# Optimization experiments

Hardware: AMD Instinct MI355X
Metric: run time of the kernel (lower is better)

## Reference

```python
import jax, jax.numpy as jnp
import numpy as np


def setup_inputs() -> dict:
    key = jax.random.key(0)
    ks = jax.random.split(key, 9)
    I, J, H, B = 1024, 1024, 32, 1024
    hid = 10
    d_in = 3 + 3 * H  # 99
    return {
        "X": jax.random.normal(ks[0], (B, I), dtype=jnp.float32),
        "weight": jax.random.normal(ks[1], (I, J), dtype=jnp.float32) * 0.1,
        "hidden_state": jax.random.normal(ks[2], (I, J, H), dtype=jnp.float32) * 0.1,
        "W1": jax.random.normal(ks[3], (d_in, hid), dtype=jnp.float32) / np.sqrt(d_in),
        "b1": jax.random.normal(ks[4], (hid,), dtype=jnp.float32) * 0.01,
        "W2": jax.random.normal(ks[5], (hid, hid), dtype=jnp.float32) / np.sqrt(hid),
        "b2": jax.random.normal(ks[6], (hid,), dtype=jnp.float32) * 0.01,
        "W3": jax.random.normal(ks[7], (hid, 1 + H), dtype=jnp.float32) / np.sqrt(hid),
        "b3": jax.random.normal(ks[8], (1 + H,), dtype=jnp.float32) * 0.01,
    }


def reference(X, weight, hidden_state, W1, b1, W2, b2, W3, b3):
    I, J = weight.shape
    H = hidden_state.shape[-1]
    # Leave-one-out means, computed once via full sums (the original recomputes
    # slice+concat+mean per cell in nested Python loops: O(I*J*(I+J)) work).
    fwd_w = (jnp.sum(weight, axis=0, keepdims=True) - weight) / (I - 1)  # (I,J) col mean excl. row i
    bwd_w = (jnp.sum(weight, axis=1, keepdims=True) - weight) / (J - 1)  # (I,J) row mean excl. col j
    fwd_h = (jnp.sum(hidden_state, axis=0, keepdims=True) - hidden_state) / (I - 1)  # (I,J,H)
    bwd_h = (jnp.sum(hidden_state, axis=1, keepdims=True) - hidden_state) / (J - 1)  # (I,J,H)
    # Per-cell feature: [w_ij, mean_fwd_w, mean_bwd_w, h_ij, mean_fwd_h, mean_bwd_h] -> (I,J,3+3H)
    feat = jnp.concatenate(
        [weight[..., None], fwd_w[..., None], bwd_w[..., None], hidden_state, fwd_h, bwd_h],
        axis=-1,
    )
    # Tiny 3-layer MLP batched over all cells (local_nn).
    h = jax.nn.relu(feat @ W1 + b1)
    h = jax.nn.relu(h @ W2 + b2)
    upd = h @ W3 + b3  # (I,J,1+H)
    new_weight = weight + upd[..., 0]
    new_hidden = hidden_state + upd[..., 1:]
    probs = jax.nn.softmax(X @ new_weight, axis=-1)  # (B,J)
    return probs, new_weight, new_hidden
```

## Files before the change

kernel.cpp:

```cpp
#include <hip/hip_runtime.h>

#define INV_I1 (1.0f/1023.0f)
#define INV_J1 (1.0f/1023.0f)

#define WS_CW     0
#define WS_RW     1024
#define WS_CH     2048
#define WS_PJT    34816
#define WS_QI     45056
#define WS_CST    55296
#define WS_LOGITS 65536
#define WS_RHP    65536
#define WS_WCP    327680
#define WS_HPART  344064

typedef __attribute__((ext_vector_type(8))) short bf16x8;
typedef __attribute__((ext_vector_type(4))) float f32x4;

__device__ inline ushort bf16_rne(float x) {
  union { float f; unsigned u; } v; v.f = x;
  unsigned r = v.u + 0x7fffu + ((v.u >> 16) & 1u);
  return (ushort)(r >> 16);
}
__device__ inline float bf16_tof(ushort h) {
  union { unsigned u; float f; } c; c.u = ((unsigned)h) << 16;
  return c.f;
}

__global__ __launch_bounds__(512) void k_red1(const float* __restrict__ Hd,
                                              float* __restrict__ hpart,
                                              float* __restrict__ rhpart,
                                              int npart) {
  __shared__ float4 s4[512];
  int t = threadIdx.x;
  int wv = t >> 6, lane = t & 63;
  int p = blockIdx.x >> 3, c = blockIdx.x & 7;
  int R = 1024 / npart;
  int i0 = p * R;
  float4 ca0 = make_float4(0.f,0.f,0.f,0.f);
  float4 ca1 = make_float4(0.f,0.f,0.f,0.f);
  for (int g = 0; g < R; g += 8) {
    #pragma unroll
    for (int r = 0; r < 8; r++) {
      int i = i0 + g + r;
      const float4* rowc = (const float4*)(Hd + (size_t)i * 32768 + c * 4096);
      float4 v0 = rowc[t];
      float4 v1 = rowc[t + 512];
      ca0.x += v0.x; ca0.y += v0.y; ca0.z += v0.z; ca0.w += v0.w;
      ca1.x += v1.x; ca1.y += v1.y; ca1.z += v1.z; ca1.w += v1.w;
      float4 rs;
      rs.x = v0.x + v1.x; rs.y = v0.y + v1.y;
      rs.z = v0.z + v1.z; rs.w = v0.w + v1.w;
      #pragma unroll
      for (int off = 8; off <= 32; off <<= 1) {
        rs.x += __shfl_xor(rs.x, off, 64);
        rs.y += __shfl_xor(rs.y, off, 64);
        rs.z += __shfl_xor(rs.z, off, 64);
        rs.w += __shfl_xor(rs.w, off, 64);
      }
      if (lane < 8) s4[(r * 8 + wv) * 8 + lane] = rs;
    }
    __syncthreads();
    if (t < 64) {
      int r = t >> 3, ln = t & 7;
      float4 a = s4[(r * 8 + 0) * 8 + ln];
      #pragma unroll
      for (int w2 = 1; w2 < 8; w2++) {
        float4 b = s4[(r * 8 + w2) * 8 + ln];
        a.x += b.x; a.y += b.y; a.z += b.z; a.w += b.w;
      }
      int i = i0 + g + r;
      ((float4*)rhpart)[i * 64 + c * 8 + ln] = a;
    }
    __syncthreads();
  }
  float4* hp = (float4*)(hpart + (size_t)p * 32768 + c * 4096);
  hp[t] = ca0;
  hp[t + 512] = ca1;
}

__global__ __launch_bounds__(256) void k_wred(const float* __restrict__ W,
                                              const float* __restrict__ X,
                                              float* __restrict__ ws,
                                              float* __restrict__ wcp,
                                              ushort* __restrict__ Xb) {
  int b = blockIdx.x, t = threadIdx.x;
  if (b < 128) {
    int wv = t >> 6, lane = t & 63;
    #pragma unroll
    for (int rr = 0; rr < 2; rr++) {
      int row = b * 8 + wv * 2 + rr;
      float acc = 0.f;
      #pragma unroll
      for (int m = 0; m < 16; m++) acc += W[row * 1024 + lane + 64 * m];
      #pragma unroll
      for (int off = 32; off > 0; off >>= 1) acc += __shfl_down(acc, off, 64);
      if (lane == 0) ws[WS_RW + row] = acc;
    }
  } else if (b < 144) {
    int p = b - 128;
    float a0 = 0.f, a1 = 0.f, a2 = 0.f, a3 = 0.f;
    for (int i = p * 64; i < p * 64 + 64; i++) {
      const float* row = W + (size_t)i * 1024;
      a0 += row[t]; a1 += row[t + 256]; a2 += row[t + 512]; a3 += row[t + 768];
    }
    wcp[p * 1024 + t] = a0;       wcp[p * 1024 + t + 256] = a1;
    wcp[p * 1024 + t + 512] = a2; wcp[p * 1024 + t + 768] = a3;
  } else {
    int g = (b - 144) * 256 + t;
    float4 v0 = ((const float4*)X)[g * 2];
    float4 v1 = ((const float4*)X)[g * 2 + 1];
    float xs[8] = {v0.x, v0.y, v0.z, v0.w, v1.x, v1.y, v1.z, v1.w};
    ushort hi[8], lo[8];
    #pragma unroll
    for (int e = 0; e < 8; e++) {
      hi[e] = bf16_rne(xs[e]);
      lo[e] = bf16_rne(xs[e] - bf16_tof(hi[e]));
    }
    ((uint4*)Xb)[g] = *(uint4*)hi;
    ((uint4*)(Xb + 1048576))[g] = *(uint4*)lo;
  }
}

__global__ __launch_bounds__(256) void k_red2pq(const float* __restrict__ hpart,
                                                const float* __restrict__ wcp,
                                                const float* __restrict__ rhpart,
                                                const float* __restrict__ W1,
                                                const float* __restrict__ b1,
                                                const float* __restrict__ W2,
                                                const float* __restrict__ b2,
                                                const float* __restrict__ W3,
                                                const float* __restrict__ b3,
                                                float* __restrict__ ws, int npart) {
  int b = blockIdx.x, t = threadIdx.x;
  if (b < 128) {
    __shared__ float chl[256];
    __shared__ float cwl[8];
    int col = b * 256 + t;
    float acc = 0.f;
    for (int p = 0; p < npart; p++) acc += hpart[(size_t)p * 32768 + col];
    ws[WS_CH + col] = acc;
    chl[t] = acc;
    if (t < 8) {
      int j = b * 8 + t;
      float a = 0.f;
      #pragma unroll
      for (int p = 0; p < 16; p++) a += wcp[p * 1024 + j];
      ws[WS_CW + j] = a;
      cwl[t] = a;
    }
    __syncthreads();
    if (t < 80) {
      int jj = t / 10, q = t - jj * 10;
      int j = b * 8 + jj;
      float o = cwl[jj] * INV_I1 * W1[10 + q];
      for (int k = 0; k < 32; k++)
        o += chl[jj * 32 + k] * INV_I1 * W1[(35 + k) * 10 + q];
      ws[WS_PJT + q * 1024 + j] = o;
    }
  } else if (b < 132) {
    int i = (b - 128) * 256 + t;
    float rh[32];
    #pragma unroll
    for (int k = 0; k < 32; k++) rh[k] = 0.f;
    for (int c = 0; c < 8; c++) {
      #pragma unroll
      for (int k = 0; k < 32; k++) rh[k] += rhpart[i * 256 + c * 32 + k];
    }
    float sr = ws[WS_RW + i] * INV_J1;
    float out[10];
    #pragma unroll
    for (int q = 0; q < 10; q++) out[q] = b1[q] + sr * W1[20 + q];
    for (int k = 0; k < 32; k++) {
      float cc = rh[k] * INV_J1;
      #pragma unroll
      for (int q = 0; q < 10; q++) out[q] += cc * W1[(67 + k) * 10 + q];
    }
    #pragma unroll
    for (int q = 0; q < 10; q++) ws[WS_QI + i * 10 + q] = out[q];
  } else {
    for (int idx = t; idx < 330; idx += 256) {
      int r = idx / 10, q = idx - r * 10;
      float v;
      if (r == 0)
        v = W1[q] - W1[10 + q] * INV_I1 - W1[20 + q] * INV_J1;
      else
        v = W1[(2 + r) * 10 + q] - W1[(34 + r) * 10 + q] * INV_I1 - W1[(66 + r) * 10 + q] * INV_J1;
      ws[WS_CST + idx] = v;
    }
    for (int idx = t; idx < 100; idx += 256) ws[WS_CST + 330 + idx] = W2[idx];
    for (int idx = t; idx < 330; idx += 256) {
      int o = idx / 10, q2 = idx - o * 10;
      ws[WS_CST + 430 + idx] = W3[q2 * 33 + o];
    }
    if (t < 10) ws[WS_CST + 760 + t] = b2[t];
    if (t < 33) ws[WS_CST + 770 + t] = b3[t];
  }
}

__global__ __launch_bounds__(256) void k_mlp(
    const float* __restrict__ W, const float* __restrict__ Hd,
    const float* __restrict__ ws,
    float* __restrict__ newW, float* __restrict__ newH) {
  __shared__ __align__(16) float hbuf[8192];
  int t = threadIdx.x;
  int cell0 = blockIdx.x * 256;
  int i = blockIdx.x >> 2;
  int j0 = (blockIdx.x & 3) * 256;
  const float* cst = ws + WS_CST;

  const float4* src = (const float4*)(Hd + (size_t)cell0 * 32);
  #pragma unroll
  for (int m = 0; m < 8; m++) {
    int s = t + 256 * m;
    float4 v = src[s];
    int cs = s >> 3, ms = s & 7;
    int slot = cs * 8 + ((ms + cs) & 7);
    *(float4*)&hbuf[slot * 4] = v;
  }
  float w0 = W[cell0 + t];
  float pj[10];
  #pragma unroll
  for (int q = 0; q < 10; q++) pj[q] = ws[WS_PJT + q * 1024 + j0 + t];
  float qv[10];
  #pragma unroll
  for (int q = 0; q < 10; q++) qv[q] = ws[WS_QI + i * 10 + q];
  __syncthreads();

  float h[32];
  #pragma unroll
  for (int m = 0; m < 8; m++) {
    int slot = t * 8 + ((m + t) & 7);
    float4 v = *(const float4*)&hbuf[slot * 4];
    h[m * 4 + 0] = v.x; h[m * 4 + 1] = v.y; h[m * 4 + 2] = v.z; h[m * 4 + 3] = v.w;
  }

  float z[10];
  #pragma unroll
  for (int q = 0; q < 10; q++) z[q] = pj[q] + qv[q] + w0 * cst[q];
  #pragma unroll
  for (int k = 0; k < 32; k++) {
    #pragma unroll
    for (int q = 0; q < 10; q++) z[q] += h[k] * cst[(k + 1) * 10 + q];
  }
  #pragma unroll
  for (int q = 0; q < 10; q++) z[q] = fmaxf(z[q], 0.f);

  float y[10];
  #pragma unroll
  for (int q2 = 0; q2 < 10; q2++) y[q2] = cst[760 + q2];
  #pragma unroll
  for (int q = 0; q < 10; q++) {
    #pragma unroll
    for (int q2 = 0; q2 < 10; q2++) y[q2] += z[q] * cst[330 + q * 10 + q2];
  }
  #pragma unroll
  for (int q2 = 0; q2 < 10; q2++) y[q2] = fmaxf(y[q2], 0.f);

  float u = cst[770];
  #pragma unroll
  for (int q2 = 0; q2 < 10; q2++) u += y[q2] * cst[430 + q2];
  newW[cell0 + t] = w0 + u;

  #pragma unroll
  for (int o = 1; o < 33; o++) {
    float a = cst[770 + o];
    #pragma unroll
    for (int q2 = 0; q2 < 10; q2++) a += y[q2] * cst[430 + o * 10 + q2];
    h[o - 1] += a;
  }

  #pragma unroll
  for (int m = 0; m < 8; m++) {
    int slot = t * 8 + ((m + t) & 7);
    *(float4*)&hbuf[slot * 4] = make_float4(h[m * 4], h[m * 4 + 1], h[m * 4 + 2], h[m * 4 + 3]);
  }
  __syncthreads();
  float4* dst = (float4*)(newH + (size_t)cell0 * 32);
  #pragma unroll
  for (int m = 0; m < 8; m++) {
    int s = t + 256 * m;
    int cs = s >> 3, ms = s & 7;
    int slot = cs * 8 + ((ms + cs) & 7);
    dst[s] = *(const float4*)&hbuf[slot * 4];
  }
}

__global__ __launch_bounds__(256) void k_wt(const float* __restrict__ nW,
                                            ushort* __restrict__ Wt) {
  __shared__ float buf[64][65];
  int t = threadIdx.x;
  int i0 = blockIdx.y * 64, j0 = blockIdx.x * 64;
  int jl = t & 63, rr = t >> 6;
  #pragma unroll
  for (int r2 = 0; r2 < 16; r2++) {
    int il = r2 * 4 + rr;
    buf[jl][il] = nW[(size_t)(i0 + il) * 1024 + j0 + jl];
  }
  __syncthreads();
  int jw = t >> 2, iq = (t & 3) * 16;
  ushort hi[16], lo[16];
  #pragma unroll
  for (int e = 0; e < 16; e++) {
    float x = buf[jw][iq + e];
    ushort h = bf16_rne(x);
    hi[e] = h;
    lo[e] = bf16_rne(x - bf16_tof(h));
  }
  size_t base = (size_t)(j0 + jw) * 1024 + i0 + iq;
  *(uint4*)(Wt + base)     = *(uint4*)hi;
  *(uint4*)(Wt + base + 8) = *(uint4*)(hi + 8);
  *(uint4*)(Wt + 1048576 + base)     = *(uint4*)lo;
  *(uint4*)(Wt + 1048576 + base + 8) = *(uint4*)(lo + 8);
}

__global__ __launch_bounds__(256) void k_gemm(const ushort* __restrict__ Xb,
                                              const ushort* __restrict__ Wt,
                                              float* __restrict__ C) {
  int t = threadIdx.x;
  int w = t >> 6, l = t & 63;
  int m0 = blockIdx.y * 64 + (w >> 1) * 32;
  int n0 = blockIdx.x * 64 + (w & 1) * 32;
  int lr = l & 15;
  int kg = (l >> 4) * 8;
  const ushort* Xhi = Xb;
  const ushort* Xlo = Xb + 1048576;
  const ushort* Whi = Wt;
  const ushort* Wlo = Wt + 1048576;
  const size_t ra0 = (size_t)(m0 + lr) * 1024;
  const size_t ra1 = (size_t)(m0 + 16 + lr) * 1024;
  const size_t cb0 = (size_t)(n0 + lr) * 1024;
  const size_t cb1 = (size_t)(n0 + 16 + lr) * 1024;
  f32x4 acc00 = {0.f, 0.f, 0.f, 0.f};
  f32x4 acc01 = {0.f, 0.f, 0.f, 0.f};
  f32x4 acc10 = {0.f, 0.f, 0.f, 0.f};
  f32x4 acc11 = {0.f, 0.f, 0.f, 0.f};
  #pragma unroll 2
  for (int k0 = 0; k0 < 1024; k0 += 32) {
    int o = k0 + kg;
    bf16x8 ah0 = *(const bf16x8*)(Xhi + ra0 + o);
    bf16x8 ah1 = *(const bf16x8*)(Xhi + ra1 + o);
    bf16x8 al0 = *(const bf16x8*)(Xlo + ra0 + o);
    bf16x8 al1 = *(const bf16x8*)(Xlo + ra1 + o);
    bf16x8 bh0 = *(const bf16x8*)(Whi + cb0 + o);
    bf16x8 bh1 = *(const bf16x8*)(Whi + cb1 + o);
    bf16x8 bl0 = *(const bf16x8*)(Wlo + cb0 + o);
    bf16x8 bl1 = *(const bf16x8*)(Wlo + cb1 + o);
    acc00 = __builtin_amdgcn_mfma_f32_16x16x32_bf16(ah0, bh0, acc00, 0, 0, 0);
    acc01 = __builtin_amdgcn_mfma_f32_16x16x32_bf16(ah0, bh1, acc01, 0, 0, 0);
    acc10 = __builtin_amdgcn_mfma_f32_16x16x32_bf16(ah1, bh0, acc10, 0, 0, 0);
    acc11 = __builtin_amdgcn_mfma_f32_16x16x32_bf16(ah1, bh1, acc11, 0, 0, 0);
    acc00 = __builtin_amdgcn_mfma_f32_16x16x32_bf16(ah0, bl0, acc00, 0, 0, 0);
    acc01 = __builtin_amdgcn_mfma_f32_16x16x32_bf16(ah0, bl1, acc01, 0, 0, 0);
    acc10 = __builtin_amdgcn_mfma_f32_16x16x32_bf16(ah1, bl0, acc10, 0, 0, 0);
    acc11 = __builtin_amdgcn_mfma_f32_16x16x32_bf16(ah1, bl1, acc11, 0, 0, 0);
    acc00 = __builtin_amdgcn_mfma_f32_16x16x32_bf16(al0, bh0, acc00, 0, 0, 0);
    acc01 = __builtin_amdgcn_mfma_f32_16x16x32_bf16(al0, bh1, acc01, 0, 0, 0);
    acc10 = __builtin_amdgcn_mfma_f32_16x16x32_bf16(al1, bh0, acc10, 0, 0, 0);
    acc11 = __builtin_amdgcn_mfma_f32_16x16x32_bf16(al1, bh1, acc11, 0, 0, 0);
  }
  int rbase = m0 + (l >> 4) * 4;
  #pragma unroll
  for (int r = 0; r < 4; r++) {
    C[(size_t)(rbase + r) * 1024 + n0 + lr]           = acc00[r];
    C[(size_t)(rbase + r) * 1024 + n0 + 16 + lr]      = acc01[r];
    C[(size_t)(rbase + 16 + r) * 1024 + n0 + lr]      = acc10[r];
    C[(size_t)(rbase + 16 + r) * 1024 + n0 + 16 + lr] = acc11[r];
  }
}

__global__ __launch_bounds__(256) void k_softmax(const float* __restrict__ L,
                                                 float* __restrict__ P) {
  __shared__ float sm[4], ss[4];
  int r = blockIdx.x, t = threadIdx.x;
  const float* row = L + r * 1024;
  float v0 = row[t], v1 = row[t + 256], v2 = row[t + 512], v3 = row[t + 768];
  float m = fmaxf(fmaxf(v0, v1), fmaxf(v2, v3));
  #pragma unroll
  for (int off = 32; off > 0; off >>= 1) m = fmaxf(m, __shfl_xor(m, off, 64));
  int wv = t >> 6, lane = t & 63;
  if (lane == 0) sm[wv] = m;
  __syncthreads();
  m = fmaxf(fmaxf(sm[0], sm[1]), fmaxf(sm[2], sm[3]));
  float e0 = expf(v0 - m), e1 = expf(v1 - m), e2 = expf(v2 - m), e3 = expf(v3 - m);
  float s = e0 + e1 + e2 + e3;
  #pragma unroll
  for (int off = 32; off > 0; off >>= 1) s += __shfl_xor(s, off, 64);
  if (lane == 0) ss[wv] = s;
  __syncthreads();
  s = ss[0] + ss[1] + ss[2] + ss[3];
  float inv = 1.0f / s;
  float* prow = P + r * 1024;
  prow[t] = e0 * inv; prow[t + 256] = e1 * inv;
  prow[t + 512] = e2 * inv; prow[t + 768] = e3 * inv;
}

extern "C" void kernel_launch(void* const* d_in, const int* in_sizes, int n_in,
                              void* d_out, int out_size, void* d_ws, size_t ws_size,
                              hipStream_t stream) {
  const float* X  = (const float*)d_in[0];
  const float* W  = (const float*)d_in[1];
  const float* Hd = (const float*)d_in[2];
  const float* W1 = (const float*)d_in[3];
  const float* b1 = (const float*)d_in[4];
  const float* W2 = (const float*)d_in[5];
  const float* b2 = (const float*)d_in[6];
  const float* W3 = (const float*)d_in[7];
  const float* b3 = (const float*)d_in[8];
  float* out   = (float*)d_out;
  float* probs = out;
  float* newW  = out + 1024 * 1024;
  float* newH  = out + 2 * 1024 * 1024;
  float* ws = (float*)d_ws;

  size_t wsf = ws_size / 4;
  int npart = 64;
  while (npart > 8 &&
         (size_t)WS_HPART + (size_t)npart * 32768ull + 2097152ull > wsf)
    npart >>= 1;
  float*  rhpart = ws + WS_RHP;
  float*  wcp    = ws + WS_WCP;
  float*  hpart  = ws + WS_HPART;
  size_t  xb0    = (size_t)WS_HPART + (size_t)npart * 32768ull;
  ushort* Xb     = (ushort*)(ws + xb0);
  ushort* Wt     = (ushort*)(ws + xb0 + 1048576);

  k_red1<<<npart * 8, 512, 0, stream>>>(Hd, hpart, rhpart, npart);
  k_wred<<<656, 256, 0, stream>>>(W, X, ws, wcp, Xb);
  k_red2pq<<<133, 256, 0, stream>>>(hpart, wcp, rhpart, W1, b1, W2, b2, W3, b3,
                                    ws, npart);
  k_mlp<<<4096, 256, 0, stream>>>(W, Hd, ws, newW, newH);
  k_wt<<<dim3(16, 16), 256, 0, stream>>>(newW, Wt);
  k_gemm<<<dim3(16, 16), 256, 0, stream>>>(Xb, Wt, ws + WS_LOGITS);
  k_softmax<<<1024, 256, 0, stream>>>(ws + WS_LOGITS, probs);
}
```

Measured before the change: 157.1 us.

## Fuse all stages into one cooperative persistent kernel with grid syncs

Replaces the seven-kernel pipeline with a single cooperative kernel of 512 blocks that runs reductions, MLP, transpose, GEMM and softmax in phases separated by grid.sync. The aim is to remove per-kernel launch gaps and tail effects between the many small stages. In exchange the kernel is capped at 512 blocks, which changes the work split of each phase (for example, the GEMM tiles shrink to 32x64 and the MLP loops over 8 tiles per block). Grid barriers also add sync cost. The previous multi-kernel path stays as a fallback when cooperative launch is not possible.

```diff
diff --git a/kernel.cpp b/kernel.cpp
--- a/kernel.cpp
+++ b/kernel.cpp
@@ -1,4 +1,7 @@
 #include <hip/hip_runtime.h>
+#include <hip/hip_cooperative_groups.h>
+
+namespace cg = cooperative_groups;
 
 #define INV_I1 (1.0f/1023.0f)
 #define INV_J1 (1.0f/1023.0f)
@@ -9,10 +12,14 @@
 #define WS_PJT    34816
 #define WS_QI     45056
 #define WS_CST    55296
-#define WS_LOGITS 65536
-#define WS_RHP    65536
-#define WS_WCP    327680
-#define WS_HPART  344064
+#define MG_RHP    65536
+#define MG_WCP    327680
+#define MG_HPART  344064
+#define MG_LOGITS 344064
+#define MG_WT     1392640
+#define MG_XB     2441216
+#define MG_TOTAL  3489792
+#define FB_LOGITS 65536
 
 typedef __attribute__((ext_vector_type(8))) short bf16x8;
 typedef __attribute__((ext_vector_type(4))) float f32x4;
@@ -25,6 +32,369 @@
 __device__ inline float bf16_tof(ushort h) {
   union { unsigned u; float f; } c; c.u = ((unsigned)h) << 16;
   return c.f;
+}
+
+__global__ __launch_bounds__(256, 2) void mega(
+    const float* __restrict__ X, const float* __restrict__ W,
+    const float* __restrict__ Hd, const float* __restrict__ W1,
+    const float* __restrict__ b1, const float* __restrict__ W2,
+    const float* __restrict__ b2, const float* __restrict__ W3,
+    const float* __restrict__ b3, float* __restrict__ out,
+    float* __restrict__ ws) {
+  __shared__ __align__(16) float smem[8192];
+  cg::grid_group grid = cg::this_grid();
+  const int blk = blockIdx.x;
+  const int t = threadIdx.x;
+  const int wv = t >> 6, lane = t & 63;
+
+  float* probs = out;
+  float* newW  = out + 1048576;
+  float* newH  = out + 2097152;
+  float* rhpart = ws + MG_RHP;
+  float* wcp    = ws + MG_WCP;
+  float* hpart  = ws + MG_HPART;
+  ushort* Xb    = (ushort*)(ws + MG_XB);
+  ushort* Wt    = (ushort*)(ws + MG_WT);
+
+  {
+    float4* s4 = (float4*)smem;
+    int p = blk >> 3, c = blk & 7;
+    int i0 = p * 16;
+    float4 ca0 = make_float4(0.f,0.f,0.f,0.f);
+    float4 ca1 = make_float4(0.f,0.f,0.f,0.f);
+    float4 ca2 = make_float4(0.f,0.f,0.f,0.f);
+    float4 ca3 = make_float4(0.f,0.f,0.f,0.f);
+    for (int g = 0; g < 16; g += 8) {
+      #pragma unroll
+      for (int r = 0; r < 8; r++) {
+        int i = i0 + g + r;
+        const float4* rowc = (const float4*)(Hd + (size_t)i * 32768 + c * 4096);
+        float4 v0 = rowc[t];
+        float4 v1 = rowc[t + 256];
+        float4 v2 = rowc[t + 512];
+        float4 v3 = rowc[t + 768];
+        ca0.x += v0.x; ca0.y += v0.y; ca0.z += v0.z; ca0.w += v0.w;
+        ca1.x += v1.x; ca1.y += v1.y; ca1.z += v1.z; ca1.w += v1.w;
+        ca2.x += v2.x; ca2.y += v2.y; ca2.z += v2.z; ca2.w += v2.w;
+        ca3.x += v3.x; ca3.y += v3.y; ca3.z += v3.z; ca3.w += v3.w;
+        float4 rs;
+        rs.x = (v0.x + v1.x) + (v2.x + v3.x);
+        rs.y = (v0.y + v1.y) + (v2.y + v3.y);
+        rs.z = (v0.z + v1.z) + (v2.z + v3.z);
+        rs.w = (v0.w + v1.w) + (v2.w + v3.w);
+        #pragma unroll
+        for (int off = 8; off <= 32; off <<= 1) {
+          rs.x += __shfl_xor(rs.x, off, 64);
+          rs.y += __shfl_xor(rs.y, off, 64);
+          rs.z += __shfl_xor(rs.z, off, 64);
+          rs.w += __shfl_xor(rs.w, off, 64);
+        }
+        if (lane < 8) s4[(r * 4 + wv) * 8 + lane] = rs;
+      }
+      __syncthreads();
+      if (t < 64) {
+        int r = t >> 3, ln = t & 7;
+        float4 a = s4[(r * 4 + 0) * 8 + ln];
+        #pragma unroll
+        for (int w2 = 1; w2 < 4; w2++) {
+          float4 b = s4[(r * 4 + w2) * 8 + ln];
+          a.x += b.x; a.y += b.y; a.z += b.z; a.w += b.w;
+        }
+        int i = i0 + g + r;
+        ((float4*)rhpart)[i * 64 + c * 8 + ln] = a;
+      }
+      __syncthreads();
+    }
+    float4* hp = (float4*)(hpart + (size_t)p * 32768 + c * 4096);
+    hp[t]       = ca0;
+    hp[t + 256] = ca1;
+    hp[t + 512] = ca2;
+    hp[t + 768] = ca3;
+  }
+  if (blk < 128) {
+    #pragma unroll
+    for (int rr = 0; rr < 2; rr++) {
+      int row = blk * 8 + wv * 2 + rr;
+      float acc = 0.f;
+      #pragma unroll
+      for (int m = 0; m < 16; m++) acc += W[row * 1024 + lane + 64 * m];
+      #pragma unroll
+      for (int off = 32; off > 0; off >>= 1) acc += __shfl_down(acc, off, 64);
+      if (lane == 0) ws[WS_RW + row] = acc;
+    }
+  } else if (blk < 144) {
+    int p2 = blk - 128;
+    float a0 = 0.f, a1 = 0.f, a2 = 0.f, a3 = 0.f;
+    for (int i = p2 * 64; i < p2 * 64 + 64; i++) {
+      const float* row = W + (size_t)i * 1024;
+      a0 += row[t]; a1 += row[t + 256]; a2 += row[t + 512]; a3 += row[t + 768];
+    }
+    wcp[p2 * 1024 + t] = a0;       wcp[p2 * 1024 + t + 256] = a1;
+    wcp[p2 * 1024 + t + 512] = a2; wcp[p2 * 1024 + t + 768] = a3;
+  }
+  {
+    int g = blk * 256 + t;
+    float4 v0 = ((const float4*)X)[g * 2];
+    float4 v1 = ((const float4*)X)[g * 2 + 1];
+    float xs[8] = {v0.x, v0.y, v0.z, v0.w, v1.x, v1.y, v1.z, v1.w};
+    ushort hi[8], lo[8];
+    #pragma unroll
+    for (int e = 0; e < 8; e++) {
+      hi[e] = bf16_rne(xs[e]);
+      lo[e] = bf16_rne(xs[e] - bf16_tof(hi[e]));
+    }
+    ((uint4*)Xb)[g] = *(uint4*)hi;
+    ((uint4*)(Xb + 1048576))[g] = *(uint4*)lo;
+  }
+  grid.sync();
+
+  if (blk < 128) {
+    float* chl = smem;
+    float* cwl = smem + 256;
+    int col = blk * 256 + t;
+    float acc = 0.f;
+    for (int p = 0; p < 64; p++) acc += hpart[(size_t)p * 32768 + col];
+    ws[WS_CH + col] = acc;
+    chl[t] = acc;
+    if (t < 8) {
+      int j = blk * 8 + t;
+      float a = 0.f;
+      #pragma unroll
+      for (int p = 0; p < 16; p++) a += wcp[p * 1024 + j];
+      ws[WS_CW + j] = a;
+      cwl[t] = a;
+    }
+    __syncthreads();
+    if (t < 80) {
+      int jj = t / 10, q = t - jj * 10;
+      int j = blk * 8 + jj;
+      float o = cwl[jj] * INV_I1 * W1[10 + q];
+      for (int k = 0; k < 32; k++)
+        o += chl[jj * 32 + k] * INV_I1 * W1[(35 + k) * 10 + q];
+      ws[WS_PJT + q * 1024 + j] = o;
+    }
+  } else if (blk < 132) {
+    int i = (blk - 128) * 256 + t;
+    float rh[32];
+    #pragma unroll
+    for (int k = 0; k < 32; k++) rh[k] = 0.f;
+    for (int c = 0; c < 8; c++) {
+      #pragma unroll
+      for (int k = 0; k < 32; k++) rh[k] += rhpart[i * 256 + c * 32 + k];
+    }
+    float sr = ws[WS_RW + i] * INV_J1;
+    float o[10];
+    #pragma unroll
+    for (int q = 0; q < 10; q++) o[q] = b1[q] + sr * W1[20 + q];
+    for (int k = 0; k < 32; k++) {
+      float cc = rh[k] * INV_J1;
+      #pragma unroll
+      for (int q = 0; q < 10; q++) o[q] += cc * W1[(67 + k) * 10 + q];
+    }
+    #pragma unroll
+    for (int q = 0; q < 10; q++) ws[WS_QI + i * 10 + q] = o[q];
+  } else if (blk == 132) {
+    for (int idx = t; idx < 330; idx += 256) {
+      int r = idx / 10, q = idx - r * 10;
+      float v;
+      if (r == 0)
+        v = W1[q] - W1[10 + q] * INV_I1 - W1[20 + q] * INV_J1;
+      else
+        v = W1[(2 + r) * 10 + q] - W1[(34 + r) * 10 + q] * INV_I1 - W1[(66 + r) * 10 + q] * INV_J1;
+      ws[WS_CST + idx] = v;
+    }
+    for (int idx = t; idx < 100; idx += 256) ws[WS_CST + 330 + idx] = W2[idx];
+    for (int idx = t; idx < 330; idx += 256) {
+      int o = idx / 10, q2 = idx - o * 10;
+      ws[WS_CST + 430 + idx] = W3[q2 * 33 + o];
+    }
+    if (t < 10) ws[WS_CST + 760 + t] = b2[t];
+    if (t < 33) ws[WS_CST + 770 + t] = b3[t];
+  }
+  grid.sync();
+
+  {
+    const float* cst = ws + WS_CST;
+    for (int g = 0; g < 8; g++) {
+      int T = g * 512 + blk;
+      int i = T >> 2;
+      int j0 = (T & 3) * 256;
+      size_t cell0 = (size_t)T * 256;
+
+      const float4* src = (const float4*)(Hd + cell0 * 32);
+      #pragma unroll
+      for (int m = 0; m < 8; m++) {
+        int s = t + 256 * m;
+        float4 v = src[s];
+        int cs = s >> 3, ms = s & 7;
+        int slot = cs * 8 + ((ms + cs) & 7);
+        *(float4*)&smem[slot * 4] = v;
+      }
+      float w0 = W[cell0 + t];
+      float pj[10];
+      #pragma unroll
+      for (int q = 0; q < 10; q++) pj[q] = ws[WS_PJT + q * 1024 + j0 + t];
+      float qv[10];
+      #pragma unroll
+      for (int q = 0; q < 10; q++) qv[q] = ws[WS_QI + i * 10 + q];
+      __syncthreads();
+
+      float h[32];
+      #pragma unroll
+      for (int m = 0; m < 8; m++) {
+        int slot = t * 8 + ((m + t) & 7);
+        float4 v = *(const float4*)&smem[slot * 4];
+        h[m * 4 + 0] = v.x; h[m * 4 + 1] = v.y; h[m * 4 + 2] = v.z; h[m * 4 + 3] = v.w;
+      }
+
+      float z[10];
+      #pragma unroll
+      for (int q = 0; q < 10; q++) z[q] = pj[q] + qv[q] + w0 * cst[q];
+      #pragma unroll
+      for (int k = 0; k < 32; k++) {
+        #pragma unroll
+        for (int q = 0; q < 10; q++) z[q] += h[k] * cst[(k + 1) * 10 + q];
+      }
+      #pragma unroll
+      for (int q = 0; q < 10; q++) z[q] = fmaxf(z[q], 0.f);
+
+      float y[10];
+      #pragma unroll
+      for (int q2 = 0; q2 < 10; q2++) y[q2] = cst[760 + q2];
+      #pragma unroll
+      for (int q = 0; q < 10; q++) {
+        #pragma unroll
+        for (int q2 = 0; q2 < 10; q2++) y[q2] += z[q] * cst[330 + q * 10 + q2];
+      }
+      #pragma unroll
+      for (int q2 = 0; q2 < 10; q2++) y[q2] = fmaxf(y[q2], 0.f);
+
+      float u = cst[770];
+      #pragma unroll
+      for (int q2 = 0; q2 < 10; q2++) u += y[q2] * cst[430 + q2];
+      newW[cell0 + t] = w0 + u;
+
+      #pragma unroll
+      for (int o = 1; o < 33; o++) {
+        float a = cst[770 + o];
+        #pragma unroll
+        for (int q2 = 0; q2 < 10; q2++) a += y[q2] * cst[430 + o * 10 + q2];
+        h[o - 1] += a;
+      }
+
+      #pragma unroll
+      for (int m = 0; m < 8; m++) {
+        int slot = t * 8 + ((m + t) & 7);
+        *(float4*)&smem[slot * 4] = make_float4(h[m*4], h[m*4+1], h[m*4+2], h[m*4+3]);
+      }
+      __syncthreads();
+      float4* dst = (float4*)(newH + cell0 * 32);
+      #pragma unroll
+      for (int m = 0; m < 8; m++) {
+        int s = t + 256 * m;
+        int cs = s >> 3, ms = s & 7;
+        int slot = cs * 8 + ((ms + cs) & 7);
+        dst[s] = *(const float4*)&smem[slot * 4];
+      }
+      __syncthreads();
+    }
+  }
+  grid.sync();
+
+  {
+    float* buf = smem;
+    int bi = blk >> 4, bj = blk & 15;
+    int i0 = bi * 32, j0 = bj * 64;
+    #pragma unroll
+    for (int r = 0; r < 8; r++) {
+      int idx = r * 256 + t;
+      int il = idx >> 6, jl = idx & 63;
+      buf[jl * 33 + il] = newW[(size_t)(i0 + il) * 1024 + j0 + jl];
+    }
+    __syncthreads();
+    int jw = t >> 2, iq = (t & 3) * 8;
+    ushort hi[8], lo[8];
+    #pragma unroll
+    for (int e = 0; e < 8; e++) {
+      float x = buf[jw * 33 + iq + e];
+      ushort hh = bf16_rne(x);
+      hi[e] = hh;
+      lo[e] = bf16_rne(x - bf16_tof(hh));
+    }
+    size_t base = (size_t)(j0 + jw) * 1024 + i0 + iq;
+    *(uint4*)(Wt + base) = *(uint4*)hi;
+    *(uint4*)(Wt + 1048576 + base) = *(uint4*)lo;
+    __syncthreads();
+  }
+  grid.sync();
+
+  {
+    float* C = ws + MG_LOGITS;
+    int bm = blk >> 4, bn = blk & 15;
+    int l = lane;
+    int mw = bm * 32 + (wv >> 1) * 16;
+    int nw = bn * 64 + (wv & 1) * 32;
+    int lr = l & 15;
+    int kg = (l >> 4) * 8;
+    const ushort* Xhi = Xb;
+    const ushort* Xlo = Xb + 1048576;
+    const ushort* Whi = Wt;
+    const ushort* Wlo = Wt + 1048576;
+    size_t ra  = (size_t)(mw + lr) * 1024;
+    size_t cb0 = (size_t)(nw + lr) * 1024;
+    size_t cb1 = (size_t)(nw + 16 + lr) * 1024;
+    f32x4 acc0 = {0.f, 0.f, 0.f, 0.f};
+    f32x4 acc1 = {0.f, 0.f, 0.f, 0.f};
+    #pragma unroll 2
+    for (int k0 = 0; k0 < 1024; k0 += 32) {
+      int o = k0 + kg;
+      bf16x8 ah  = *(const bf16x8*)(Xhi + ra + o);
+      bf16x8 al  = *(const bf16x8*)(Xlo + ra + o);
+      bf16x8 bh0 = *(const bf16x8*)(Whi + cb0 + o);
+      bf16x8 bl0 = *(const bf16x8*)(Wlo + cb0 + o);
+      bf16x8 bh1 = *(const bf16x8*)(Whi + cb1 + o);
+      bf16x8 bl1 = *(const bf16x8*)(Wlo + cb1 + o);
+      acc0 = __builtin_amdgcn_mfma_f32_16x16x32_bf16(ah, bh0, acc0, 0, 0, 0);
+      acc1 = __builtin_amdgcn_mfma_f32_16x16x32_bf16(ah, bh1, acc1, 0, 0, 0);
+      acc0 = __builtin_amdgcn_mfma_f32_16x16x32_bf16(ah, bl0, acc0, 0, 0, 0);
+      acc1 = __builtin_amdgcn_mfma_f32_16x16x32_bf16(ah, bl1, acc1, 0, 0, 0);
+      acc0 = __builtin_amdgcn_mfma_f32_16x16x32_bf16(al, bh0, acc0, 0, 0, 0);
+      acc1 = __builtin_amdgcn_mfma_f32_16x16x32_bf16(al, bh1, acc1, 0, 0, 0);
+    }
+    int rbase = mw + (l >> 4) * 4;
+    #pragma unroll
+    for (int r = 0; r < 4; r++) {
+      C[(size_t)(rbase + r) * 1024 + nw + lr]      = acc0[r];
+      C[(size_t)(rbase + r) * 1024 + nw + 16 + lr] = acc1[r];
+    }
+  }
+  grid.sync();
+
+  for (int it = 0; it < 2; it++) {
+    float* sm = smem;
+    float* ss = smem + 4;
+    int r = it * 512 + blk;
+    const float* row = ws + MG_LOGITS + (size_t)r * 1024;
+    float v0 = row[t], v1 = row[t + 256], v2 = row[t + 512], v3 = row[t + 768];
+    float m = fmaxf(fmaxf(v0, v1), fmaxf(v2, v3));
+    #pragma unroll
+    for (int off = 32; off > 0; off >>= 1) m = fmaxf(m, __shfl_xor(m, off, 64));
+    if (lane == 0) sm[wv] = m;
+    __syncthreads();
+    m = fmaxf(fmaxf(sm[0], sm[1]), fmaxf(sm[2], sm[3]));
+    float e0 = expf(v0 - m), e1 = expf(v1 - m), e2 = expf(v2 - m), e3 = expf(v3 - m);
+    float s = e0 + e1 + e2 + e3;
+    #pragma unroll
+    for (int off = 32; off > 0; off >>= 1) s += __shfl_xor(s, off, 64);
+    if (lane == 0) ss[wv] = s;
+    __syncthreads();
+    s = ss[0] + ss[1] + ss[2] + ss[3];
+    float inv = 1.0f / s;
+    float* prow = probs + (size_t)r * 1024;
+    prow[t] = e0 * inv;       prow[t + 256] = e1 * inv;
+    prow[t + 512] = e2 * inv; prow[t + 768] = e3 * inv;
+    __syncthreads();
+  }
 }
 
 __global__ __launch_bounds__(512) void k_red1(const float* __restrict__ Hd,
@@ -403,25 +773,49 @@
   const float* Hd = (const float*)d_in[2];
   const float* W1 = (const float*)d_in[3];
   const float* b1 = (const float*)d_in[4];
+  const float* b1_ = b1;
   const float* W2 = (const float*)d_in[5];
   const float* b2 = (const float*)d_in[6];
   const float* W3 = (const float*)d_in[7];
   const float* b3 = (const float*)d_in[8];
-  float* out   = (float*)d_out;
+  float* out = (float*)d_out;
+  float* ws  = (float*)d_ws;
+
+  bool coop_ok = false;
+  if (ws_size / 4 >= (size_t)MG_TOTAL) {
+    int maxBlk = 0;
+    if (hipOccupancyMaxActiveBlocksPerMultiprocessor(&maxBlk, mega, 256, 0) ==
+        hipSuccess) {
+      int dev = 0;
+      hipGetDevice(&dev);
+      hipDeviceProp_t prop;
+      if (hipGetDeviceProperties(&prop, dev) == hipSuccess &&
+          (long long)maxBlk * prop.multiProcessorCount >= 512)
+        coop_ok = true;
+    }
+  }
+
+  if (coop_ok) {
+    void* args[] = {(void*)&X, (void*)&W, (void*)&Hd, (void*)&W1, (void*)&b1_,
+                    (void*)&W2, (void*)&b2, (void*)&W3, (void*)&b3,
+                    (void*)&out, (void*)&ws};
+    hipLaunchCooperativeKernel((void*)mega, dim3(512), dim3(256), args, 0,
+                               stream);
+    return;
+  }
+
   float* probs = out;
-  float* newW  = out + 1024 * 1024;
-  float* newH  = out + 2 * 1024 * 1024;
-  float* ws = (float*)d_ws;
-
+  float* newW  = out + 1048576;
+  float* newH  = out + 2097152;
   size_t wsf = ws_size / 4;
   int npart = 64;
   while (npart > 8 &&
-         (size_t)WS_HPART + (size_t)npart * 32768ull + 2097152ull > wsf)
+         (size_t)MG_HPART + (size_t)npart * 32768ull + 2097152ull > wsf)
     npart >>= 1;
-  float*  rhpart = ws + WS_RHP;
-  float*  wcp    = ws + WS_WCP;
-  float*  hpart  = ws + WS_HPART;
-  size_t  xb0    = (size_t)WS_HPART + (size_t)npart * 32768ull;
+  float*  rhpart = ws + MG_RHP;
+  float*  wcp    = ws + MG_WCP;
+  float*  hpart  = ws + MG_HPART;
+  size_t  xb0    = (size_t)MG_HPART + (size_t)npart * 32768ull;
   ushort* Xb     = (ushort*)(ws + xb0);
   ushort* Wt     = (ushort*)(ws + xb0 + 1048576);
 
@@ -431,6 +825,6 @@
                                     ws, npart);
   k_mlp<<<4096, 256, 0, stream>>>(W, Hd, ws, newW, newH);
   k_wt<<<dim3(16, 16), 256, 0, stream>>>(newW, Wt);
-  k_gemm<<<dim3(16, 16), 256, 0, stream>>>(Xb, Wt, ws + WS_LOGITS);
-  k_softmax<<<1024, 256, 0, stream>>>(ws + WS_LOGITS, probs);
-}
+  k_gemm<<<dim3(16, 16), 256, 0, stream>>>(Xb, Wt, ws + FB_LOGITS);
+  k_softmax<<<1024, 256, 0, stream>>>(ws + FB_LOGITS, probs);
+}
```

After: 158.4 us. Within noise of the previous version (+0.8%).

## Fuse hidden-state and weight reduction kernels into one launch, use nontemporal stores

Applied to the files above, without the earlier changes.

Merges the hidden-state partial reduction kernel and the weight row/column sum plus X bf16 split kernel into a single 512-thread launch with block-range dispatch, so the small weight work can overlap the large streaming reduction and one launch is removed. Block-to-work mappings are adjusted for 512 threads (row sums use one row per wave, column partials use two columns per thread, X conversion uses 512 elements per block). The newH writes in the MLP kernel and the probability writes in softmax switch to nontemporal stores to avoid polluting cache with write-once output. The fused kernel mixes heterogeneous block types, which can cause tail imbalance.

```diff
diff --git a/kernel.cpp b/kernel.cpp
--- a/kernel.cpp
+++ b/kernel.cpp
@@ -27,87 +27,89 @@
   return c.f;
 }
 
-__global__ __launch_bounds__(512) void k_red1(const float* __restrict__ Hd,
-                                              float* __restrict__ hpart,
-                                              float* __restrict__ rhpart,
-                                              int npart) {
+__device__ inline void nt_store4(float* p, float a, float b, float c, float d) {
+  f32x4 v = {a, b, c, d};
+  __builtin_nontemporal_store(v, (f32x4*)p);
+}
+
+__global__ __launch_bounds__(512) void k_pass1(const float* __restrict__ W,
+                                               const float* __restrict__ X,
+                                               const float* __restrict__ Hd,
+                                               float* __restrict__ ws,
+                                               float* __restrict__ hpart,
+                                               float* __restrict__ wcp,
+                                               ushort* __restrict__ Xb,
+                                               int npart) {
   __shared__ float4 s4[512];
   int t = threadIdx.x;
   int wv = t >> 6, lane = t & 63;
-  int p = blockIdx.x >> 3, c = blockIdx.x & 7;
-  int R = 1024 / npart;
-  int i0 = p * R;
-  float4 ca0 = make_float4(0.f,0.f,0.f,0.f);
-  float4 ca1 = make_float4(0.f,0.f,0.f,0.f);
-  for (int g = 0; g < R; g += 8) {
-    #pragma unroll
-    for (int r = 0; r < 8; r++) {
-      int i = i0 + g + r;
-      const float4* rowc = (const float4*)(Hd + (size_t)i * 32768 + c * 4096);
-      float4 v0 = rowc[t];
-      float4 v1 = rowc[t + 512];
-      ca0.x += v0.x; ca0.y += v0.y; ca0.z += v0.z; ca0.w += v0.w;
-      ca1.x += v1.x; ca1.y += v1.y; ca1.z += v1.z; ca1.w += v1.w;
-      float4 rs;
-      rs.x = v0.x + v1.x; rs.y = v0.y + v1.y;
-      rs.z = v0.z + v1.z; rs.w = v0.w + v1.w;
+  int blk = blockIdx.x;
+  int nred = npart * 8;
+  float* rhpart = ws + WS_RHP;
+
+  if (blk < nred) {
+    int p = blk >> 3, c = blk & 7;
+    int R = 1024 / npart;
+    int i0 = p * R;
+    float4 ca0 = make_float4(0.f,0.f,0.f,0.f);
+    float4 ca1 = make_float4(0.f,0.f,0.f,0.f);
+    for (int g = 0; g < R; g += 8) {
       #pragma unroll
-      for (int off = 8; off <= 32; off <<= 1) {
-        rs.x += __shfl_xor(rs.x, off, 64);
-        rs.y += __shfl_xor(rs.y, off, 64);
-        rs.z += __shfl_xor(rs.z, off, 64);
-        rs.w += __shfl_xor(rs.w, off, 64);
+      for (int r = 0; r < 8; r++) {
+        int i = i0 + g + r;
+        const float4* rowc = (const float4*)(Hd + (size_t)i * 32768 + c * 4096);
+        float4 v0 = rowc[t];
+        float4 v1 = rowc[t + 512];
+        ca0.x += v0.x; ca0.y += v0.y; ca0.z += v0.z; ca0.w += v0.w;
+        ca1.x += v1.x; ca1.y += v1.y; ca1.z += v1.z; ca1.w += v1.w;
+        float4 rs;
+        rs.x = v0.x + v1.x; rs.y = v0.y + v1.y;
+        rs.z = v0.z + v1.z; rs.w = v0.w + v1.w;
+        #pragma unroll
+        for (int off = 8; off <= 32; off <<= 1) {
+          rs.x += __shfl_xor(rs.x, off, 64);
+          rs.y += __shfl_xor(rs.y, off, 64);
+          rs.z += __shfl_xor(rs.z, off, 64);
+          rs.w += __shfl_xor(rs.w, off, 64);
+        }
+        if (lane < 8) s4[(r * 8 + wv) * 8 + lane] = rs;
       }
-      if (lane < 8) s4[(r * 8 + wv) * 8 + lane] = rs;
-    }
-    __syncthreads();
-    if (t < 64) {
-      int r = t >> 3, ln = t & 7;
-      float4 a = s4[(r * 8 + 0) * 8 + ln];
-      #pragma unroll
-      for (int w2 = 1; w2 < 8; w2++) {
-        float4 b = s4[(r * 8 + w2) * 8 + ln];
-        a.x += b.x; a.y += b.y; a.z += b.z; a.w += b.w;
+      __syncthreads();
+      if (t < 64) {
+        int r = t >> 3, ln = t & 7;
+        float4 a = s4[(r * 8 + 0) * 8 + ln];
+        #pragma unroll
+        for (int w2 = 1; w2 < 8; w2++) {
+          float4 b = s4[(r * 8 + w2) * 8 + ln];
+          a.x += b.x; a.y += b.y; a.z += b.z; a.w += b.w;
+        }
+        int i = i0 + g + r;
+        ((float4*)rhpart)[i * 64 + c * 8 + ln] = a;
       }
-      int i = i0 + g + r;
-      ((float4*)rhpart)[i * 64 + c * 8 + ln] = a;
-    }
-    __syncthreads();
-  }
-  float4* hp = (float4*)(hpart + (size_t)p * 32768 + c * 4096);
-  hp[t] = ca0;
-  hp[t + 512] = ca1;
-}
-
-__global__ __launch_bounds__(256) void k_wred(const float* __restrict__ W,
-                                              const float* __restrict__ X,
-                                              float* __restrict__ ws,
-                                              float* __restrict__ wcp,
-                                              ushort* __restrict__ Xb) {
-  int b = blockIdx.x, t = threadIdx.x;
-  if (b < 128) {
-    int wv = t >> 6, lane = t & 63;
-    #pragma unroll
-    for (int rr = 0; rr < 2; rr++) {
-      int row = b * 8 + wv * 2 + rr;
-      float acc = 0.f;
-      #pragma unroll
-      for (int m = 0; m < 16; m++) acc += W[row * 1024 + lane + 64 * m];
-      #pragma unroll
-      for (int off = 32; off > 0; off >>= 1) acc += __shfl_down(acc, off, 64);
-      if (lane == 0) ws[WS_RW + row] = acc;
-    }
-  } else if (b < 144) {
-    int p = b - 128;
-    float a0 = 0.f, a1 = 0.f, a2 = 0.f, a3 = 0.f;
-    for (int i = p * 64; i < p * 64 + 64; i++) {
+      __syncthreads();
+    }
+    float4* hp = (float4*)(hpart + (size_t)p * 32768 + c * 4096);
+    hp[t] = ca0;
+    hp[t + 512] = ca1;
+  } else if (blk < nred + 128) {
+    int row = (blk - nred) * 8 + wv;
+    float acc = 0.f;
+    #pragma unroll
+    for (int m = 0; m < 16; m++) acc += W[row * 1024 + lane + 64 * m];
+    #pragma unroll
+    for (int off = 32; off > 0; off >>= 1) acc += __shfl_down(acc, off, 64);
+    if (lane == 0) ws[WS_RW + row] = acc;
+  } else if (blk < nred + 144) {
+    int p2 = blk - nred - 128;
+    float a0 = 0.f, a1 = 0.f;
+    for (int i = p2 * 64; i < p2 * 64 + 64; i++) {
       const float* row = W + (size_t)i * 1024;
-      a0 += row[t]; a1 += row[t + 256]; a2 += row[t + 512]; a3 += row[t + 768];
-    }
-    wcp[p * 1024 + t] = a0;       wcp[p * 1024 + t + 256] = a1;
-    wcp[p * 1024 + t + 512] = a2; wcp[p * 1024 + t + 768] = a3;
+      a0 += row[t]; a1 += row[t + 512];
+    }
+    wcp[p2 * 1024 + t] = a0;
+    wcp[p2 * 1024 + t + 512] = a1;
   } else {
-    int g = (b - 144) * 256 + t;
+    int g = (blk - nred - 144) * 512 + t;
     float4 v0 = ((const float4*)X)[g * 2];
     float4 v1 = ((const float4*)X)[g * 2 + 1];
     float xs[8] = {v0.x, v0.y, v0.z, v0.w, v1.x, v1.y, v1.z, v1.w};
@@ -276,13 +278,14 @@
     *(float4*)&hbuf[slot * 4] = make_float4(h[m * 4], h[m * 4 + 1], h[m * 4 + 2], h[m * 4 + 3]);
   }
   __syncthreads();
-  float4* dst = (float4*)(newH + (size_t)cell0 * 32);
+  float* dstf = newH + (size_t)cell0 * 32;
   #pragma unroll
   for (int m = 0; m < 8; m++) {
     int s = t + 256 * m;
     int cs = s >> 3, ms = s & 7;
     int slot = cs * 8 + ((ms + cs) & 7);
-    dst[s] = *(const float4*)&hbuf[slot * 4];
+    const float* hv = &hbuf[slot * 4];
+    nt_store4(dstf + s * 4, hv[0], hv[1], hv[2], hv[3]);
   }
 }
 
@@ -391,8 +394,10 @@
   s = ss[0] + ss[1] + ss[2] + ss[3];
   float inv = 1.0f / s;
   float* prow = P + r * 1024;
-  prow[t] = e0 * inv; prow[t + 256] = e1 * inv;
-  prow[t + 512] = e2 * inv; prow[t + 768] = e3 * inv;
+  __builtin_nontemporal_store(e0 * inv, &prow[t]);
+  __builtin_nontemporal_store(e1 * inv, &prow[t + 256]);
+  __builtin_nontemporal_store(e2 * inv, &prow[t + 512]);
+  __builtin_nontemporal_store(e3 * inv, &prow[t + 768]);
 }
 
 extern "C" void kernel_launch(void* const* d_in, const int* in_sizes, int n_in,
@@ -409,8 +414,8 @@
   const float* b3 = (const float*)d_in[8];
   float* out   = (float*)d_out;
   float* probs = out;
-  float* newW  = out + 1024 * 1024;
-  float* newH  = out + 2 * 1024 * 1024;
+  float* newW  = out + 1048576;
+  float* newH  = out + 2097152;
   float* ws = (float*)d_ws;
 
   size_t wsf = ws_size / 4;
@@ -425,8 +430,8 @@
   ushort* Xb     = (ushort*)(ws + xb0);
   ushort* Wt     = (ushort*)(ws + xb0 + 1048576);
 
-  k_red1<<<npart * 8, 512, 0, stream>>>(Hd, hpart, rhpart, npart);
-  k_wred<<<656, 256, 0, stream>>>(W, X, ws, wcp, Xb);
+  k_pass1<<<npart * 8 + 400, 512, 0, stream>>>(W, X, Hd, ws, hpart, wcp, Xb,
+                                               npart);
   k_red2pq<<<133, 256, 0, stream>>>(hpart, wcp, rhpart, W1, b1, W2, b2, W3, b3,
                                     ws, npart);
   k_mlp<<<4096, 256, 0, stream>>>(W, Hd, ws, newW, newH);
```

Result: faster. 152.5 us, median of 2 (-2.9%).
